# Kernel tuning notes

Measured on AMD Instinct MI355X. Metric: run time of the kernel, lower is better.

Reference implementation:

```python
import jax, jax.numpy as jnp
import numpy as np

D_MODEL = 1024
NUM_HEADS = 16
D_K = D_MODEL // NUM_HEADS
SCALE = 1.0 / np.sqrt(D_K).astype(np.float32)
NEG_INF = -1.0e9


def setup_inputs() -> dict:
    key = jax.random.key(0)
    ks = jax.random.split(key, 9)
    B, S = 4, 2048
    query = jax.random.normal(ks[0], (B, S, D_MODEL), dtype=jnp.float32)
    key_t = jax.random.normal(ks[1], (B, S, D_MODEL), dtype=jnp.float32)
    value = jax.random.normal(ks[2], (B, S, D_MODEL), dtype=jnp.float32)
    mask = jax.random.randint(ks[3], (B, S), 0, 2, dtype=jnp.int32)
    init = 1.0 / np.sqrt(D_MODEL).astype(np.float32)
    W_q = jax.random.uniform(ks[4], (D_MODEL, D_MODEL), jnp.float32, -init, init)
    W_k = jax.random.uniform(ks[5], (D_MODEL, D_MODEL), jnp.float32, -init, init)
    W_v = jax.random.uniform(ks[6], (D_MODEL, D_MODEL), jnp.float32, -init, init)
    W_o = jax.random.uniform(ks[7], (D_MODEL, D_MODEL), jnp.float32, -init, init)
    b_o = jax.random.uniform(ks[8], (D_MODEL,), jnp.float32, -init, init)
    return {"query": query, "key": key_t, "value": value, "mask": mask,
            "W_q": W_q, "W_k": W_k, "W_v": W_v, "W_o": W_o, "b_o": b_o}


def reference(query, key, value, mask, W_q, W_k, W_v, W_o, b_o):
    B, S, _ = query.shape
    # projections -> [B, H, S, d_k]  (torch Linear: x @ W.T)
    def split_heads(x, W):
        y = jnp.einsum('bsd,ed->bse', x, W)
        return y.reshape(B, S, NUM_HEADS, D_K).transpose(0, 2, 1, 3)
    Q = split_heads(query, W_q)
    K = split_heads(key, W_k)
    V = split_heads(value, W_v)
    # scores [B, H, S, S]
    scores = jnp.einsum('bhqd,bhkd->bhqk', Q, K) * SCALE
    key_mask = (mask[:, None, None, :] != 0)  # [B,1,1,S] over key axis
    scores = jnp.where(key_mask, scores, NEG_INF)
    probs = jax.nn.softmax(scores, axis=-1)
    # dropout is identity (p=0 / eval mode)
    context = jnp.einsum('bhqk,bhkd->bhqd', probs, V)
    context = context.transpose(0, 2, 1, 3).reshape(B, S, D_MODEL)
    output = jnp.einsum('bsd,ed->bse', context, W_o) + b_o
    return output, probs.mean(axis=1)
```

## Files before the change

kernel.cpp:

```cpp
#include <hip/hip_runtime.h>

typedef unsigned short u16t;
typedef __bf16 bf16x8 __attribute__((ext_vector_type(8)));
typedef float f32x4 __attribute__((ext_vector_type(4)));

#define NB 4
#define NS 2048
#define ND 1024
#define NH 16
#define NDK 64
#define NEGINF -1.0e9f
#define SCALE2 0.18033688011112042f

#define LAB 40

__device__ __forceinline__ float fexp2(float x) { return __builtin_amdgcn_exp2f(x); }

__device__ __forceinline__ u16t f2bf(float f) {
  return __builtin_bit_cast(u16t, (__bf16)f);
}

#define ROR16(x, n) __builtin_bit_cast(float, __builtin_amdgcn_update_dpp(     \
    __builtin_bit_cast(int, (x)), __builtin_bit_cast(int, (x)),                \
    0x120 + (n), 0xF, 0xF, false))

__device__ __forceinline__ int swz(int row, int col) {
  return row * 64 + (col ^ ((row & 7) << 3));
}

template<typename TA> struct Stg;
template<> struct Stg<float> {
  f32x4 lo, hi;
  __device__ __forceinline__ void ld(const float* p) {
    lo = *(const f32x4*)p; hi = *(const f32x4*)(p + 4);
  }
  __device__ __forceinline__ bf16x8 get() const {
    bf16x8 r;
    r[0] = (__bf16)lo[0]; r[1] = (__bf16)lo[1]; r[2] = (__bf16)lo[2]; r[3] = (__bf16)lo[3];
    r[4] = (__bf16)hi[0]; r[5] = (__bf16)hi[1]; r[6] = (__bf16)hi[2]; r[7] = (__bf16)hi[3];
    return r;
  }
};
template<> struct Stg<u16t> {
  bf16x8 v;
  __device__ __forceinline__ void ld(const u16t* p) { v = *(const bf16x8*)p; }
  __device__ __forceinline__ bf16x8 get() const { return v; }
};

template<typename TA, int MODE>
__global__ __launch_bounds__(256, 2)
void gemm_nt(const TA* __restrict__ A, const float* __restrict__ Bm,
             void* __restrict__ Cv, const float* __restrict__ bias)
{
  const int K = 1024;
  __shared__ __attribute__((aligned(16))) u16t At[128 * LAB];
  __shared__ __attribute__((aligned(16))) u16t Bt[128 * LAB];

  const int tid  = threadIdx.x;
  const int w    = tid >> 6;
  const int lane = tid & 63;
  const int quad = lane >> 4;
  const int l16  = lane & 15;
  const int wm   = w >> 1, wn = w & 1;
  const int m0   = blockIdx.x * 128;
  const int n0   = blockIdx.y * 128;

  const f32x4 fz = {0.f, 0.f, 0.f, 0.f};
  f32x4 acc[4][4];
#pragma unroll
  for (int i = 0; i < 4; i++)
#pragma unroll
    for (int j = 0; j < 4; j++) acc[i][j] = fz;

  const int r0 = tid >> 2, cg = (tid & 3) * 8;
  const int r1 = r0 + 64;

  Stg<TA> sa0, sa1; Stg<float> sb0, sb1;
  sa0.ld(A  + (long)(m0 + r0) * K + cg);
  sa1.ld(A  + (long)(m0 + r1) * K + cg);
  sb0.ld(Bm + (long)(n0 + r0) * K + cg);
  sb1.ld(Bm + (long)(n0 + r1) * K + cg);

  for (int k0 = 0; k0 < K; k0 += 32) {
    __syncthreads();
    *(bf16x8*)&At[r0 * LAB + cg] = sa0.get();
    *(bf16x8*)&At[r1 * LAB + cg] = sa1.get();
    *(bf16x8*)&Bt[r0 * LAB + cg] = sb0.get();
    *(bf16x8*)&Bt[r1 * LAB + cg] = sb1.get();
    __syncthreads();
    if (k0 + 32 < K) {
      sa0.ld(A  + (long)(m0 + r0) * K + k0 + 32 + cg);
      sa1.ld(A  + (long)(m0 + r1) * K + k0 + 32 + cg);
      sb0.ld(Bm + (long)(n0 + r0) * K + k0 + 32 + cg);
      sb1.ld(Bm + (long)(n0 + r1) * K + k0 + 32 + cg);
    }

    bf16x8 af[4], bfv[4];
#pragma unroll
    for (int i = 0; i < 4; i++)
      af[i] = *(const bf16x8*)&At[(wm * 64 + i * 16 + l16) * LAB + quad * 8];
#pragma unroll
    for (int j = 0; j < 4; j++)
      bfv[j] = *(const bf16x8*)&Bt[(wn * 64 + j * 16 + l16) * LAB + quad * 8];
#pragma unroll
    for (int i = 0; i < 4; i++)
#pragma unroll
      for (int j = 0; j < 4; j++)
        acc[i][j] = __builtin_amdgcn_mfma_f32_16x16x32_bf16(af[i], bfv[j], acc[i][j], 0, 0, 0);
  }

#pragma unroll
  for (int i = 0; i < 4; i++) {
    const int rbase = m0 + wm * 64 + i * 16 + quad * 4;
#pragma unroll
    for (int j = 0; j < 4; j++) {
      const int col = n0 + wn * 64 + j * 16 + l16;
      float bv = 0.f;
      if (MODE == 0) bv = bias[col];
#pragma unroll
      for (int r = 0; r < 4; r++) {
        const int row = rbase + r;
        float v = acc[i][j][r];
        if (MODE == 0) {
          ((float*)Cv)[(long)row * ND + col] = v + bv;
        } else if (MODE == 1) {
          int b = row >> 11, s = row & 2047, h = col >> 6, d = col & 63;
          ((u16t*)Cv)[(((long)(b * NH + h)) * NS + s) * NDK + d] = f2bf(v);
        } else {
          int b = row >> 11, s = row & 2047, h = col >> 6, d = col & 63;
          ((u16t*)Cv)[(((long)(b * NH + h)) * NDK + d) * NS + s] = f2bf(v);
        }
      }
    }
  }
}

__global__ __launch_bounds__(256, 4)
void flash_ctx(const u16t* __restrict__ Qw, const u16t* __restrict__ Kw,
               const u16t* __restrict__ VTw, const int* __restrict__ mask,
               u16t* __restrict__ ctx, float* __restrict__ mo, float* __restrict__ lo)
{
  __shared__ __attribute__((aligned(16))) u16t Kt[64 * 64];
  __shared__ __attribute__((aligned(16))) u16t Vt[64 * 64];
  __shared__ __attribute__((aligned(16))) u16t Pt[4 * 16 * 64];
  __shared__ float biasl[NS];

  const int tid  = threadIdx.x;
  const int w    = tid >> 6;
  const int lane = tid & 63;
  const int quad = lane >> 4;
  const int l16  = lane & 15;
  const int bh   = blockIdx.y;
  const int b    = bh >> 4;
  const int h    = bh & 15;
  const int qw   = blockIdx.x * 128 + w * 32;
  const int pbase = w * 1024;

  for (int i = tid; i < NS; i += 256)
    biasl[i] = mask[b * NS + i] ? 0.f : NEGINF;

  bf16x8 qf[2][2];
#pragma unroll
  for (int g = 0; g < 2; g++)
#pragma unroll
    for (int kk = 0; kk < 2; kk++)
      qf[g][kk] = *(const bf16x8*)(Qw + ((long)bh * NS + qw + g * 16 + l16) * NDK + kk * 32 + quad * 8);

  const f32x4 fz = {0.f, 0.f, 0.f, 0.f};
  const f32x4 fm = {NEGINF, NEGINF, NEGINF, NEGINF};
  f32x4 cacc[2][4];
#pragma unroll
  for (int g = 0; g < 2; g++)
#pragma unroll
    for (int d = 0; d < 4; d++) cacc[g][d] = fz;
  f32x4 mrun[2] = {fm, fm};
  f32x4 lrun[2] = {fz, fz};

  const int kr0 = tid >> 3, kc0 = (tid & 7) * 8;
  const int kr1 = kr0 + 32;
  const long kbase = (long)bh * NS;
  const long vbase = (long)bh * NDK;

  bf16x8 k0v = *(const bf16x8*)(Kw  + (kbase + kr0) * NDK + kc0);
  bf16x8 k1v = *(const bf16x8*)(Kw  + (kbase + kr1) * NDK + kc0);
  bf16x8 v0v = *(const bf16x8*)(VTw + (vbase + kr0) * NS + kc0);
  bf16x8 v1v = *(const bf16x8*)(VTw + (vbase + kr1) * NS + kc0);

  for (int kb = 0; kb < NS; kb += 64) {
    __syncthreads();
    *(bf16x8*)&Kt[swz(kr0, kc0)] = k0v;
    *(bf16x8*)&Kt[swz(kr1, kc0)] = k1v;
    *(bf16x8*)&Vt[swz(kr0, kc0)] = v0v;
    *(bf16x8*)&Vt[swz(kr1, kc0)] = v1v;
    __syncthreads();
    if (kb + 64 < NS) {
      k0v = *(const bf16x8*)(Kw  + (kbase + kb + 64 + kr0) * NDK + kc0);
      k1v = *(const bf16x8*)(Kw  + (kbase + kb + 64 + kr1) * NDK + kc0);
      v0v = *(const bf16x8*)(VTw + (vbase + kr0) * NS + kb + 64 + kc0);
      v1v = *(const bf16x8*)(VTw + (vbase + kr1) * NS + kb + 64 + kc0);
    }

    float bias_c[4];
#pragma unroll
    for (int c = 0; c < 4; c++) bias_c[c] = biasl[kb + c * 16 + l16];

#pragma unroll
    for (int g = 0; g < 2; g++) {
      f32x4 s[4];
#pragma unroll
      for (int c = 0; c < 4; c++) {
        f32x4 a = fz;
#pragma unroll
        for (int kk = 0; kk < 2; kk++) {
          bf16x8 kf = *(const bf16x8*)&Kt[swz(c * 16 + l16, kk * 32 + quad * 8)];
          a = __builtin_amdgcn_mfma_f32_16x16x32_bf16(qf[g][kk], kf, a, 0, 0, 0);
        }
        s[c] = a;
      }

#pragma unroll
      for (int c = 0; c < 4; c++)
#pragma unroll
        for (int r = 0; r < 4; r++)
          s[c][r] = s[c][r] * SCALE2 + bias_c[c];

      f32x4 mx = s[0];
#pragma unroll
      for (int c = 1; c < 4; c++)
#pragma unroll
        for (int r = 0; r < 4; r++) mx[r] = fmaxf(mx[r], s[c][r]);
#pragma unroll
      for (int r = 0; r < 4; r++) {
        float x = mx[r];
        x = fmaxf(x, ROR16(x, 1));
        x = fmaxf(x, ROR16(x, 2));
        x = fmaxf(x, ROR16(x, 4));
        x = fmaxf(x, ROR16(x, 8));
        mx[r] = x;
      }

      f32x4 alpha;
#pragma unroll
      for (int r = 0; r < 4; r++) {
        float mnew = fmaxf(mrun[g][r], mx[r]);
        alpha[r] = fexp2(mrun[g][r] - mnew);
        mrun[g][r] = mnew;
      }
#pragma unroll
      for (int c = 0; c < 4; c++)
#pragma unroll
        for (int r = 0; r < 4; r++) s[c][r] = fexp2(s[c][r] - mrun[g][r]);

      f32x4 sm = fz;
#pragma unroll
      for (int c = 0; c < 4; c++)
#pragma unroll
        for (int r = 0; r < 4; r++) sm[r] += s[c][r];
#pragma unroll
      for (int r = 0; r < 4; r++) {
        float x = sm[r];
        x += ROR16(x, 1);
        x += ROR16(x, 2);
        x += ROR16(x, 4);
        x += ROR16(x, 8);
        sm[r] = x;
      }
#pragma unroll
      for (int r = 0; r < 4; r++) lrun[g][r] = lrun[g][r] * alpha[r] + sm[r];
#pragma unroll
      for (int d = 0; d < 4; d++)
#pragma unroll
        for (int r = 0; r < 4; r++) cacc[g][d][r] *= alpha[r];

#pragma unroll
      for (int c = 0; c < 4; c++)
#pragma unroll
        for (int r = 0; r < 4; r++)
          Pt[pbase + swz(quad * 4 + r, c * 16 + l16)] = f2bf(s[c][r]);

#pragma unroll
      for (int d = 0; d < 4; d++)
#pragma unroll
        for (int kk = 0; kk < 2; kk++) {
          bf16x8 pf = *(const bf16x8*)&Pt[pbase + swz(l16, kk * 32 + quad * 8)];
          bf16x8 vf = *(const bf16x8*)&Vt[swz(d * 16 + l16, kk * 32 + quad * 8)];
          cacc[g][d] = __builtin_amdgcn_mfma_f32_16x16x32_bf16(pf, vf, cacc[g][d], 0, 0, 0);
        }
    }
  }

#pragma unroll
  for (int g = 0; g < 2; g++) {
    f32x4 rinv;
#pragma unroll
    for (int r = 0; r < 4; r++) rinv[r] = 1.f / lrun[g][r];
#pragma unroll
    for (int d = 0; d < 4; d++)
#pragma unroll
      for (int r = 0; r < 4; r++) {
        int qg = qw + g * 16 + quad * 4 + r;
        int e  = h * NDK + d * 16 + l16;
        ctx[((long)(b * NS + qg)) * ND + e] = f2bf(cacc[g][d][r] * rinv[r]);
      }
    if (l16 == 0) {
#pragma unroll
      for (int r = 0; r < 4; r++) {
        int qg = qw + g * 16 + quad * 4 + r;
        mo[(long)bh * NS + qg] = mrun[g][r];
        lo[(long)bh * NS + qg] = lrun[g][r];
      }
    }
  }
}

__global__ __launch_bounds__(256, 3)
void probs_mean(const u16t* __restrict__ Qw, const u16t* __restrict__ Kw,
                const int* __restrict__ mask, const float* __restrict__ mo,
                const float* __restrict__ lo, float* __restrict__ outp)
{
  __shared__ __attribute__((aligned(16))) u16t Qt[128 * 64];
  __shared__ __attribute__((aligned(16))) u16t Kt2[128 * 64];
  __shared__ float ml[NH * 128];
  __shared__ float li[NH * 128];
  __shared__ float biasl[128];

  const int tid  = threadIdx.x;
  const int w    = tid >> 6;
  const int lane = tid & 63;
  const int quad = lane >> 4;
  const int l16  = lane & 15;
  const int wm   = w >> 1, wn = w & 1;
  const int b  = blockIdx.z;
  const int q0 = blockIdx.y * 128;
  const int k0 = blockIdx.x * 128;

  for (int i = tid; i < NH * 128; i += 256) {
    int hh = i >> 7, r = i & 127;
    ml[i] = mo[((long)(b * NH + hh)) * NS + q0 + r];
    li[i] = 1.f / lo[((long)(b * NH + hh)) * NS + q0 + r];
  }
  for (int i = tid; i < 128; i += 256)
    biasl[i] = mask[b * NS + k0 + i] ? 0.f : NEGINF;

  const f32x4 fz = {0.f, 0.f, 0.f, 0.f};
  f32x4 acc[4][4];
#pragma unroll
  for (int i = 0; i < 4; i++)
#pragma unroll
    for (int j = 0; j < 4; j++) acc[i][j] = fz;

  bf16x8 qv[4], kv[4];
#pragma unroll
  for (int rr = 0; rr < 4; rr++) {
    int idx = rr * 256 + tid;
    int row = idx >> 3, off = (idx & 7) * 8;
    qv[rr] = *(const bf16x8*)(Qw + ((long)(b * NH) * NS + q0 + row) * NDK + off);
    kv[rr] = *(const bf16x8*)(Kw + ((long)(b * NH) * NS + k0 + row) * NDK + off);
  }

  for (int hh = 0; hh < NH; hh++) {
    __syncthreads();
#pragma unroll
    for (int rr = 0; rr < 4; rr++) {
      int idx = rr * 256 + tid;
      int row = idx >> 3, off = (idx & 7) * 8;
      *(bf16x8*)&Qt[swz(row, off)]  = qv[rr];
      *(bf16x8*)&Kt2[swz(row, off)] = kv[rr];
    }
    __syncthreads();
    if (hh + 1 < NH) {
#pragma unroll
      for (int rr = 0; rr < 4; rr++) {
        int idx = rr * 256 + tid;
        int row = idx >> 3, off = (idx & 7) * 8;
        qv[rr] = *(const bf16x8*)(Qw + ((long)(b * NH + hh + 1) * NS + q0 + row) * NDK + off);
        kv[rr] = *(const bf16x8*)(Kw + ((long)(b * NH + hh + 1) * NS + k0 + row) * NDK + off);
      }
    }

    bf16x8 af[4][2], bfv[4][2];
#pragma unroll
    for (int i = 0; i < 4; i++)
#pragma unroll
      for (int kk = 0; kk < 2; kk++) {
        af[i][kk]  = *(const bf16x8*)&Qt[swz(wm * 64 + i * 16 + l16, kk * 32 + quad * 8)];
        bfv[i][kk] = *(const bf16x8*)&Kt2[swz(wn * 64 + i * 16 + l16, kk * 32 + quad * 8)];
      }
#pragma unroll
    for (int i = 0; i < 4; i++)
#pragma unroll
      for (int j = 0; j < 4; j++) {
        f32x4 s = fz;
#pragma unroll
        for (int kk = 0; kk < 2; kk++)
          s = __builtin_amdgcn_mfma_f32_16x16x32_bf16(af[i][kk], bfv[j][kk], s, 0, 0, 0);
        const float bias_c = biasl[wn * 64 + j * 16 + l16];
#pragma unroll
        for (int r = 0; r < 4; r++) {
          int rowb = wm * 64 + i * 16 + quad * 4 + r;
          float p = fexp2(s[r] * SCALE2 + bias_c - ml[hh * 128 + rowb]) * li[hh * 128 + rowb];
          acc[i][j][r] += p;
        }
      }
  }

#pragma unroll
  for (int i = 0; i < 4; i++)
#pragma unroll
    for (int j = 0; j < 4; j++)
#pragma unroll
      for (int r = 0; r < 4; r++) {
        int row = q0 + wm * 64 + i * 16 + quad * 4 + r;
        int col = k0 + wn * 64 + j * 16 + l16;
        outp[((long)(b * NS + row)) * NS + col] = acc[i][j][r] * (1.f / 16.f);
      }
}

extern "C" void kernel_launch(void* const* d_in, const int* in_sizes, int n_in,
                              void* d_out, int out_size, void* d_ws, size_t ws_size,
                              hipStream_t stream)
{
  (void)in_sizes; (void)n_in; (void)out_size; (void)ws_size;
  const float* query = (const float*)d_in[0];
  const float* keyt  = (const float*)d_in[1];
  const float* value = (const float*)d_in[2];
  const int*   mask  = (const int*)d_in[3];
  const float* Wq = (const float*)d_in[4];
  const float* Wk = (const float*)d_in[5];
  const float* Wv = (const float*)d_in[6];
  const float* Wo = (const float*)d_in[7];
  const float* bo = (const float*)d_in[8];

  float* out  = (float*)d_out;
  float* outp = out + (long)NB * NS * ND;

  u16t* q_ws  = (u16t*)d_ws;
  u16t* k_ws  = q_ws + (long)NB * NH * NS * NDK;
  u16t* vt_ws = k_ws + (long)NB * NH * NS * NDK;
  float* m_ws = (float*)(vt_ws + (long)NB * NH * NS * NDK);
  float* l_ws = m_ws + (long)NB * NH * NS;
  u16t* ctx_ws = (u16t*)outp;

  dim3 blk(256);
  gemm_nt<float, 1><<<dim3(64, 8), blk, 0, stream>>>(query, Wq, q_ws, nullptr);
  gemm_nt<float, 1><<<dim3(64, 8), blk, 0, stream>>>(keyt,  Wk, k_ws, nullptr);
  gemm_nt<float, 2><<<dim3(64, 8), blk, 0, stream>>>(value, Wv, vt_ws, nullptr);
  flash_ctx<<<dim3(NS / 128, NB * NH), blk, 0, stream>>>(q_ws, k_ws, vt_ws, mask,
                                                         ctx_ws, m_ws, l_ws);
  gemm_nt<u16t, 0><<<dim3(64, 8), blk, 0, stream>>>(ctx_ws, Wo, out, bo);
  probs_mean<<<dim3(NS / 128, NS / 128, NB), blk, 0, stream>>>(q_ws, k_ws, mask,
                                                               m_ws, l_ws, outp);
}
```

Before: 579.0 us.

## Use 8 waves of 16 query rows each in flash attention block

The flash attention kernel moves from 4 waves each handling two 16-row query groups to 8 waves each handling one group, launched with 512 threads. The K/V tile staging is spread over twice as many threads, so each thread loads one vector instead of two, and per-wave register state (Q fragments, accumulators, running max and sum) is halved. The aim is more latency hiding and less serial work per wave. In exchange, each K/V tile loaded into shared memory is reused by fewer query rows per wave and the per-tile barrier cost is shared across more waves.

```diff
diff --git a/kernel.cpp b/kernel.cpp
--- a/kernel.cpp
+++ b/kernel.cpp
@@ -135,14 +135,14 @@
   }
 }
 
-__global__ __launch_bounds__(256, 4)
+__global__ __launch_bounds__(512, 4)
 void flash_ctx(const u16t* __restrict__ Qw, const u16t* __restrict__ Kw,
                const u16t* __restrict__ VTw, const int* __restrict__ mask,
                u16t* __restrict__ ctx, float* __restrict__ mo, float* __restrict__ lo)
 {
   __shared__ __attribute__((aligned(16))) u16t Kt[64 * 64];
   __shared__ __attribute__((aligned(16))) u16t Vt[64 * 64];
-  __shared__ __attribute__((aligned(16))) u16t Pt[4 * 16 * 64];
+  __shared__ __attribute__((aligned(16))) u16t Pt[8 * 16 * 64];
   __shared__ float biasl[NS];
 
   const int tid  = threadIdx.x;
@@ -153,161 +153,144 @@
   const int bh   = blockIdx.y;
   const int b    = bh >> 4;
   const int h    = bh & 15;
-  const int qw   = blockIdx.x * 128 + w * 32;
+  const int qw   = blockIdx.x * 128 + w * 16;
   const int pbase = w * 1024;
 
-  for (int i = tid; i < NS; i += 256)
+  for (int i = tid; i < NS; i += 512)
     biasl[i] = mask[b * NS + i] ? 0.f : NEGINF;
 
-  bf16x8 qf[2][2];
-#pragma unroll
-  for (int g = 0; g < 2; g++)
-#pragma unroll
-    for (int kk = 0; kk < 2; kk++)
-      qf[g][kk] = *(const bf16x8*)(Qw + ((long)bh * NS + qw + g * 16 + l16) * NDK + kk * 32 + quad * 8);
+  bf16x8 qf[2];
+#pragma unroll
+  for (int kk = 0; kk < 2; kk++)
+    qf[kk] = *(const bf16x8*)(Qw + ((long)bh * NS + qw + l16) * NDK + kk * 32 + quad * 8);
 
   const f32x4 fz = {0.f, 0.f, 0.f, 0.f};
   const f32x4 fm = {NEGINF, NEGINF, NEGINF, NEGINF};
-  f32x4 cacc[2][4];
-#pragma unroll
-  for (int g = 0; g < 2; g++)
-#pragma unroll
-    for (int d = 0; d < 4; d++) cacc[g][d] = fz;
-  f32x4 mrun[2] = {fm, fm};
-  f32x4 lrun[2] = {fz, fz};
+  f32x4 cacc[4];
+#pragma unroll
+  for (int d = 0; d < 4; d++) cacc[d] = fz;
+  f32x4 mrun = fm;
+  f32x4 lrun = fz;
 
   const int kr0 = tid >> 3, kc0 = (tid & 7) * 8;
-  const int kr1 = kr0 + 32;
   const long kbase = (long)bh * NS;
   const long vbase = (long)bh * NDK;
 
-  bf16x8 k0v = *(const bf16x8*)(Kw  + (kbase + kr0) * NDK + kc0);
-  bf16x8 k1v = *(const bf16x8*)(Kw  + (kbase + kr1) * NDK + kc0);
-  bf16x8 v0v = *(const bf16x8*)(VTw + (vbase + kr0) * NS + kc0);
-  bf16x8 v1v = *(const bf16x8*)(VTw + (vbase + kr1) * NS + kc0);
+  bf16x8 kv = *(const bf16x8*)(Kw  + (kbase + kr0) * NDK + kc0);
+  bf16x8 vv = *(const bf16x8*)(VTw + (vbase + kr0) * NS + kc0);
 
   for (int kb = 0; kb < NS; kb += 64) {
     __syncthreads();
-    *(bf16x8*)&Kt[swz(kr0, kc0)] = k0v;
-    *(bf16x8*)&Kt[swz(kr1, kc0)] = k1v;
-    *(bf16x8*)&Vt[swz(kr0, kc0)] = v0v;
-    *(bf16x8*)&Vt[swz(kr1, kc0)] = v1v;
+    *(bf16x8*)&Kt[swz(kr0, kc0)] = kv;
+    *(bf16x8*)&Vt[swz(kr0, kc0)] = vv;
     __syncthreads();
     if (kb + 64 < NS) {
-      k0v = *(const bf16x8*)(Kw  + (kbase + kb + 64 + kr0) * NDK + kc0);
-      k1v = *(const bf16x8*)(Kw  + (kbase + kb + 64 + kr1) * NDK + kc0);
-      v0v = *(const bf16x8*)(VTw + (vbase + kr0) * NS + kb + 64 + kc0);
-      v1v = *(const bf16x8*)(VTw + (vbase + kr1) * NS + kb + 64 + kc0);
-    }
-
-    float bias_c[4];
-#pragma unroll
-    for (int c = 0; c < 4; c++) bias_c[c] = biasl[kb + c * 16 + l16];
-
-#pragma unroll
-    for (int g = 0; g < 2; g++) {
-      f32x4 s[4];
-#pragma unroll
-      for (int c = 0; c < 4; c++) {
-        f32x4 a = fz;
-#pragma unroll
-        for (int kk = 0; kk < 2; kk++) {
-          bf16x8 kf = *(const bf16x8*)&Kt[swz(c * 16 + l16, kk * 32 + quad * 8)];
-          a = __builtin_amdgcn_mfma_f32_16x16x32_bf16(qf[g][kk], kf, a, 0, 0, 0);
-        }
-        s[c] = a;
-      }
-
-#pragma unroll
-      for (int c = 0; c < 4; c++)
-#pragma unroll
-        for (int r = 0; r < 4; r++)
-          s[c][r] = s[c][r] * SCALE2 + bias_c[c];
-
-      f32x4 mx = s[0];
-#pragma unroll
-      for (int c = 1; c < 4; c++)
-#pragma unroll
-        for (int r = 0; r < 4; r++) mx[r] = fmaxf(mx[r], s[c][r]);
+      kv = *(const bf16x8*)(Kw  + (kbase + kb + 64 + kr0) * NDK + kc0);
+      vv = *(const bf16x8*)(VTw + (vbase + kr0) * NS + kb + 64 + kc0);
+    }
+
+    f32x4 s[4];
+#pragma unroll
+    for (int c = 0; c < 4; c++) {
+      f32x4 a = fz;
+#pragma unroll
+      for (int kk = 0; kk < 2; kk++) {
+        bf16x8 kf = *(const bf16x8*)&Kt[swz(c * 16 + l16, kk * 32 + quad * 8)];
+        a = __builtin_amdgcn_mfma_f32_16x16x32_bf16(qf[kk], kf, a, 0, 0, 0);
+      }
+      s[c] = a;
+    }
+
+#pragma unroll
+    for (int c = 0; c < 4; c++) {
+      const float bias_c = biasl[kb + c * 16 + l16];
+#pragma unroll
+      for (int r = 0; r < 4; r++)
+        s[c][r] = s[c][r] * SCALE2 + bias_c;
+    }
+
+    f32x4 mx = s[0];
+#pragma unroll
+    for (int c = 1; c < 4; c++)
+#pragma unroll
+      for (int r = 0; r < 4; r++) mx[r] = fmaxf(mx[r], s[c][r]);
+#pragma unroll
+    for (int r = 0; r < 4; r++) {
+      float x = mx[r];
+      x = fmaxf(x, ROR16(x, 1));
+      x = fmaxf(x, ROR16(x, 2));
+      x = fmaxf(x, ROR16(x, 4));
+      x = fmaxf(x, ROR16(x, 8));
+      mx[r] = x;
+    }
+
+    f32x4 alpha;
+#pragma unroll
+    for (int r = 0; r < 4; r++) {
+      float mnew = fmaxf(mrun[r], mx[r]);
+      alpha[r] = fexp2(mrun[r] - mnew);
+      mrun[r] = mnew;
+    }
+#pragma unroll
+    for (int c = 0; c < 4; c++)
+#pragma unroll
+      for (int r = 0; r < 4; r++) s[c][r] = fexp2(s[c][r] - mrun[r]);
+
+    f32x4 sm = fz;
+#pragma unroll
+    for (int c = 0; c < 4; c++)
+#pragma unroll
+      for (int r = 0; r < 4; r++) sm[r] += s[c][r];
+#pragma unroll
+    for (int r = 0; r < 4; r++) {
+      float x = sm[r];
+      x += ROR16(x, 1);
+      x += ROR16(x, 2);
+      x += ROR16(x, 4);
+      x += ROR16(x, 8);
+      sm[r] = x;
+    }
+#pragma unroll
+    for (int r = 0; r < 4; r++) lrun[r] = lrun[r] * alpha[r] + sm[r];
+#pragma unroll
+    for (int d = 0; d < 4; d++)
+#pragma unroll
+      for (int r = 0; r < 4; r++) cacc[d][r] *= alpha[r];
+
+#pragma unroll
+    for (int c = 0; c < 4; c++)
+#pragma unroll
+      for (int r = 0; r < 4; r++)
+        Pt[pbase + swz(quad * 4 + r, c * 16 + l16)] = f2bf(s[c][r]);
+
+#pragma unroll
+    for (int d = 0; d < 4; d++)
+#pragma unroll
+      for (int kk = 0; kk < 2; kk++) {
+        bf16x8 pf = *(const bf16x8*)&Pt[pbase + swz(l16, kk * 32 + quad * 8)];
+        bf16x8 vf = *(const bf16x8*)&Vt[swz(d * 16 + l16, kk * 32 + quad * 8)];
+        cacc[d] = __builtin_amdgcn_mfma_f32_16x16x32_bf16(pf, vf, cacc[d], 0, 0, 0);
+      }
+  }
+
+  {
+    f32x4 rinv;
+#pragma unroll
+    for (int r = 0; r < 4; r++) rinv[r] = 1.f / lrun[r];
+#pragma unroll
+    for (int d = 0; d < 4; d++)
 #pragma unroll
       for (int r = 0; r < 4; r++) {
-        float x = mx[r];
-        x = fmaxf(x, ROR16(x, 1));
-        x = fmaxf(x, ROR16(x, 2));
-        x = fmaxf(x, ROR16(x, 4));
-        x = fmaxf(x, ROR16(x, 8));
-        mx[r] = x;
-      }
-
-      f32x4 alpha;
+        int qg = qw + quad * 4 + r;
+        int e  = h * NDK + d * 16 + l16;
+        ctx[((long)(b * NS + qg)) * ND + e] = f2bf(cacc[d][r] * rinv[r]);
+      }
+    if (l16 == 0) {
 #pragma unroll
       for (int r = 0; r < 4; r++) {
-        float mnew = fmaxf(mrun[g][r], mx[r]);
-        alpha[r] = fexp2(mrun[g][r] - mnew);
-        mrun[g][r] = mnew;
-      }
-#pragma unroll
-      for (int c = 0; c < 4; c++)
-#pragma unroll
-        for (int r = 0; r < 4; r++) s[c][r] = fexp2(s[c][r] - mrun[g][r]);
-
-      f32x4 sm = fz;
-#pragma unroll
-      for (int c = 0; c < 4; c++)
-#pragma unroll
-        for (int r = 0; r < 4; r++) sm[r] += s[c][r];
-#pragma unroll
-      for (int r = 0; r < 4; r++) {
-        float x = sm[r];
-        x += ROR16(x, 1);
-        x += ROR16(x, 2);
-        x += ROR16(x, 4);
-        x += ROR16(x, 8);
-        sm[r] = x;
-      }
-#pragma unroll
-      for (int r = 0; r < 4; r++) lrun[g][r] = lrun[g][r] * alpha[r] + sm[r];
-#pragma unroll
-      for (int d = 0; d < 4; d++)
-#pragma unroll
-        for (int r = 0; r < 4; r++) cacc[g][d][r] *= alpha[r];
-
-#pragma unroll
-      for (int c = 0; c < 4; c++)
-#pragma unroll
-        for (int r = 0; r < 4; r++)
-          Pt[pbase + swz(quad * 4 + r, c * 16 + l16)] = f2bf(s[c][r]);
-
-#pragma unroll
-      for (int d = 0; d < 4; d++)
-#pragma unroll
-        for (int kk = 0; kk < 2; kk++) {
-          bf16x8 pf = *(const bf16x8*)&Pt[pbase + swz(l16, kk * 32 + quad * 8)];
-          bf16x8 vf = *(const bf16x8*)&Vt[swz(d * 16 + l16, kk * 32 + quad * 8)];
-          cacc[g][d] = __builtin_amdgcn_mfma_f32_16x16x32_bf16(pf, vf, cacc[g][d], 0, 0, 0);
-        }
-    }
-  }
-
-#pragma unroll
-  for (int g = 0; g < 2; g++) {
-    f32x4 rinv;
-#pragma unroll
-    for (int r = 0; r < 4; r++) rinv[r] = 1.f / lrun[g][r];
-#pragma unroll
-    for (int d = 0; d < 4; d++)
-#pragma unroll
-      for (int r = 0; r < 4; r++) {
-        int qg = qw + g * 16 + quad * 4 + r;
-        int e  = h * NDK + d * 16 + l16;
-        ctx[((long)(b * NS + qg)) * ND + e] = f2bf(cacc[g][d][r] * rinv[r]);
-      }
-    if (l16 == 0) {
-#pragma unroll
-      for (int r = 0; r < 4; r++) {
-        int qg = qw + g * 16 + quad * 4 + r;
-        mo[(long)bh * NS + qg] = mrun[g][r];
-        lo[(long)bh * NS + qg] = lrun[g][r];
+        int qg = qw + quad * 4 + r;
+        mo[(long)bh * NS + qg] = mrun[r];
+        lo[(long)bh * NS + qg] = lrun[r];
       }
     }
   }
@@ -445,8 +428,8 @@
   gemm_nt<float, 1><<<dim3(64, 8), blk, 0, stream>>>(query, Wq, q_ws, nullptr);
   gemm_nt<float, 1><<<dim3(64, 8), blk, 0, stream>>>(keyt,  Wk, k_ws, nullptr);
   gemm_nt<float, 2><<<dim3(64, 8), blk, 0, stream>>>(value, Wv, vt_ws, nullptr);
-  flash_ctx<<<dim3(NS / 128, NB * NH), blk, 0, stream>>>(q_ws, k_ws, vt_ws, mask,
-                                                         ctx_ws, m_ws, l_ws);
+  flash_ctx<<<dim3(NS / 128, NB * NH), dim3(512), 0, stream>>>(q_ws, k_ws, vt_ws, mask,
+                                                               ctx_ws, m_ws, l_ws);
   gemm_nt<u16t, 0><<<dim3(64, 8), blk, 0, stream>>>(ctx_ws, Wo, out, bo);
   probs_mean<<<dim3(NS / 128, NS / 128, NB), blk, 0, stream>>>(q_ws, k_ws, mask,
                                                                m_ws, l_ws, outp);
```

Result: faster. 518.3 us (-10.5%).
